# Kernel optimization log

Hardware: AMD Instinct MI355X
Metric: run time of the kernel (lower is better)

The kernel has to match this reference:

```python
import jax, jax.numpy as jnp
import numpy as np

NUM_SEGMENTS = 512
N = 200000
D = 256


def setup_inputs() -> dict:
    key = jax.random.key(0)
    k = jax.random.split(key, 6)
    x = jax.random.normal(k[0], (N, D), dtype=jnp.float32)
    batch = jnp.sort(jax.random.randint(k[1], (N,), 0, NUM_SEGMENTS))
    batch = batch.at[-1].set(NUM_SEGMENTS - 1)  # ensure batch.max()+1 == NUM_SEGMENTS
    W1 = jax.random.normal(k[2], (D, D // 2), dtype=jnp.float32) * (1.0 / np.sqrt(D))
    b1 = jax.random.normal(k[3], (D // 2,), dtype=jnp.float32) * 0.01
    W2 = jax.random.normal(k[4], (D // 2, 1), dtype=jnp.float32) * (1.0 / np.sqrt(D // 2))
    b2 = jax.random.normal(k[5], (1,), dtype=jnp.float32) * 0.01
    return {"x": x, "batch": batch, "W1": W1, "b1": b1, "W2": W2, "b2": b2}


def reference(x, batch, W1, b1, W2, b2):
    # attention MLP: Linear -> Tanh -> Linear -> [N, 1]
    scores = (jnp.tanh(x @ W1 + b1) @ W2 + b2)[:, 0]  # [N]
    # segment softmax (numerically stable): subtract per-segment max
    smax = jax.ops.segment_max(scores, batch, num_segments=NUM_SEGMENTS)  # [G]
    e = jnp.exp(scores - smax[batch])  # [N]
    denom = jax.ops.segment_sum(e, batch, num_segments=NUM_SEGMENTS)  # [G]
    denom = jnp.where(denom > 0, denom, 1.0)  # guard empty segments (original yields zeros)
    w = e / denom[batch]  # [N]
    # weighted sum pooling per segment -> [G, D]
    return jax.ops.segment_sum(x * w[:, None], batch, num_segments=NUM_SEGMENTS)
```

## Files before the change

### kernel.cpp

```cpp
#include <hip/hip_runtime.h>
#include <math.h>


typedef __attribute__((ext_vector_type(4))) float f32x4;
typedef __attribute__((ext_vector_type(8))) short s16x8;

#define MFMA16(A, B, C) __builtin_amdgcn_mfma_f32_16x16x32_bf16((A), (B), (C), 0, 0, 0)

__device__ __forceinline__ unsigned short f2bf_rne(float f) {
    unsigned int u = __float_as_uint(f);
    unsigned int r = u + 0x7FFFu + ((u >> 16) & 1u);
    return (unsigned short)(r >> 16);
}
__device__ __forceinline__ float bf2f(unsigned short h) {
    return __uint_as_float(((unsigned int)h) << 16);
}

#define APITCH 36
#define BPITCH 40

__global__ __launch_bounds__(256)
void scores_mfma(const float* __restrict__ x, const float* __restrict__ W1,
                 const float* __restrict__ b1, const float* __restrict__ W2,
                 const float* __restrict__ b2, float* __restrict__ scores, int N)
{
    __shared__ __align__(16) float Afp[128 * APITCH];
    __shared__ __align__(16) unsigned short Bhi[128 * BPITCH];
    __shared__ __align__(16) unsigned short Blo[128 * BPITCH];

    const int tid  = threadIdx.x;
    const int wave = tid >> 6;
    const int lane = tid & 63;
    const int c    = lane & 15;
    const int q    = lane >> 4;
    const int rowBase = blockIdx.x * 128;

    f32x4 acc[2][8];
#pragma unroll
    for (int mt = 0; mt < 2; ++mt)
#pragma unroll
        for (int nt = 0; nt < 8; ++nt)
            acc[mt][nt] = (f32x4){0.f, 0.f, 0.f, 0.f};

    const int nB   = tid & 127;
    const int half = tid >> 7;

    for (int k0 = 0; k0 < 256; k0 += 32) {
        __syncthreads();
#pragma unroll
        for (int i = 0; i < 4; ++i) {
            int idx = tid + 256 * i;
            int r   = idx >> 3;
            int c4  = idx & 7;
            int row = rowBase + r;
            f32x4 v = (f32x4){0.f, 0.f, 0.f, 0.f};
            if (row < N)
                v = *(const f32x4*)(x + (size_t)row * 256 + k0 + c4 * 4);
            *(f32x4*)&Afp[r * APITCH + c4 * 4] = v;
        }
#pragma unroll
        for (int g = 0; g < 4; ++g) {
            unsigned short hs[4], ls[4];
#pragma unroll
            for (int e = 0; e < 4; ++e) {
                int kk = half * 16 + g * 4 + e;
                float f = W1[(size_t)(k0 + kk) * 128 + nB];
                unsigned short h = f2bf_rne(f);
                hs[e] = h;
                ls[e] = f2bf_rne(f - bf2f(h));
            }
            *(ushort4*)&Bhi[nB * BPITCH + half * 16 + g * 4] =
                make_ushort4(hs[0], hs[1], hs[2], hs[3]);
            *(ushort4*)&Blo[nB * BPITCH + half * 16 + g * 4] =
                make_ushort4(ls[0], ls[1], ls[2], ls[3]);
        }
        __syncthreads();

        s16x8 ahi[2], alo[2];
#pragma unroll
        for (int mt = 0; mt < 2; ++mt) {
            int m = wave * 32 + mt * 16 + c;
            f32x4 a0 = *(const f32x4*)&Afp[m * APITCH + q * 8];
            f32x4 a1 = *(const f32x4*)&Afp[m * APITCH + q * 8 + 4];
            float av[8] = {a0.x, a0.y, a0.z, a0.w, a1.x, a1.y, a1.z, a1.w};
#pragma unroll
            for (int j = 0; j < 8; ++j) {
                unsigned short h = f2bf_rne(av[j]);
                ahi[mt][j] = (short)h;
                alo[mt][j] = (short)f2bf_rne(av[j] - bf2f(h));
            }
        }
#pragma unroll
        for (int nt = 0; nt < 8; ++nt) {
            int nr = nt * 16 + c;
            s16x8 bh = *(const s16x8*)&Bhi[nr * BPITCH + q * 8];
            s16x8 bl = *(const s16x8*)&Blo[nr * BPITCH + q * 8];
#pragma unroll
            for (int mt = 0; mt < 2; ++mt) {
                acc[mt][nt] = MFMA16(ahi[mt], bh, acc[mt][nt]);
                acc[mt][nt] = MFMA16(ahi[mt], bl, acc[mt][nt]);
                acc[mt][nt] = MFMA16(alo[mt], bh, acc[mt][nt]);
            }
        }
    }

    float b1v[8], w2v[8];
#pragma unroll
    for (int nt = 0; nt < 8; ++nt) {
        b1v[nt] = b1[nt * 16 + c];
        w2v[nt] = W2[nt * 16 + c];
    }
    const float bias2 = b2[0];

#pragma unroll
    for (int mt = 0; mt < 2; ++mt) {
#pragma unroll
        for (int reg = 0; reg < 4; ++reg) {
            float p = 0.f;
#pragma unroll
            for (int nt = 0; nt < 8; ++nt) {
                float v = acc[mt][nt][reg] + b1v[nt];
                float e = __expf(2.f * v);
                p += (1.f - 2.f / (e + 1.f)) * w2v[nt];
            }
#pragma unroll
            for (int off = 8; off > 0; off >>= 1)
                p += __shfl_xor(p, off, 16);
            if (c == 0) {
                int row = rowBase + wave * 32 + mt * 16 + q * 4 + reg;
                if (row < N) scores[row] = p + bias2;
            }
        }
    }
}

__device__ __forceinline__ int lower_bound_dev(const int* __restrict__ b, int n, int v)
{
    int lo = 0, hi = n;
    while (lo < hi) {
        int mid = (lo + hi) >> 1;
        if (b[mid] < v) lo = mid + 1; else hi = mid;
    }
    return lo;
}

__global__ __launch_bounds__(1024)
void segpool_kernel(const float* __restrict__ x, const int* __restrict__ batch,
                    const float* __restrict__ scores, float* __restrict__ out, int N)
{
    const int g = blockIdx.x;
    const int tid = threadIdx.x;
    const int fidx  = tid & 63;
    const int rslot = tid >> 6;

    __shared__ int se[2];
    __shared__ float sred[1024];
    __shared__ float4 rbuf[16][64];

    if (tid < 2) se[tid] = lower_bound_dev(batch, N, g + tid);
    __syncthreads();
    const int start = se[0], end = se[1];

    float m = -INFINITY;
    for (int i = start + tid; i < end; i += 1024) m = fmaxf(m, scores[i]);
#pragma unroll
    for (int off = 32; off > 0; off >>= 1) m = fmaxf(m, __shfl_xor(m, off, 64));
    if ((tid & 63) == 0) sred[tid >> 6] = m;
    __syncthreads();
    if (tid < 16) {
        float v = sred[tid];
#pragma unroll
        for (int off = 8; off > 0; off >>= 1) v = fmaxf(v, __shfl_xor(v, off, 16));
        if (tid == 0) sred[0] = v;
    }
    __syncthreads();
    m = sred[0];
    __syncthreads();

    float ssum = 0.f;
    for (int i = start + tid; i < end; i += 1024) ssum += expf(scores[i] - m);
#pragma unroll
    for (int off = 32; off > 0; off >>= 1) ssum += __shfl_xor(ssum, off, 64);
    if ((tid & 63) == 0) sred[tid >> 6] = ssum;
    __syncthreads();
    if (tid < 16) {
        float v = sred[tid];
#pragma unroll
        for (int off = 8; off > 0; off >>= 1) v += __shfl_xor(v, off, 16);
        if (tid == 0) sred[0] = v;
    }
    __syncthreads();
    const float denom = sred[0];
    const float inv = (denom > 0.f) ? 1.f / denom : 0.f;

    float4 acc = make_float4(0.f, 0.f, 0.f, 0.f);
    for (int base = start; base < end; base += 1024) {
        int cnt = min(1024, end - base);
        __syncthreads();
        if (tid < cnt) sred[tid] = expf(scores[base + tid] - m) * inv;
        __syncthreads();
#pragma unroll 2
        for (int j = rslot; j < cnt; j += 16) {
            float w = sred[j];
            float4 v = *(const float4*)(x + (size_t)(base + j) * 256 + fidx * 4);
            acc.x = fmaf(w, v.x, acc.x);
            acc.y = fmaf(w, v.y, acc.y);
            acc.z = fmaf(w, v.z, acc.z);
            acc.w = fmaf(w, v.w, acc.w);
        }
    }

    rbuf[rslot][fidx] = acc;
    __syncthreads();
#pragma unroll
    for (int s = 8; s > 0; s >>= 1) {
        if (rslot < s) {
            float4 o = rbuf[rslot + s][fidx];
            acc.x += o.x; acc.y += o.y; acc.z += o.z; acc.w += o.w;
            rbuf[rslot][fidx] = acc;
        }
        __syncthreads();
    }
    if (rslot == 0)
        ((float4*)out)[(size_t)g * 64 + fidx] = acc;
}

extern "C" void kernel_launch(void* const* d_in, const int* in_sizes, int n_in,
                              void* d_out, int out_size, void* d_ws, size_t ws_size,
                              hipStream_t stream) {
    const float* x     = (const float*)d_in[0];
    const int*   batch = (const int*)  d_in[1];
    const float* W1    = (const float*)d_in[2];
    const float* b1    = (const float*)d_in[3];
    const float* W2    = (const float*)d_in[4];
    const float* b2    = (const float*)d_in[5];
    float* out = (float*)d_out;

    const int N = in_sizes[1];
    const int G = out_size / 256;

    float* scores = (float*)d_ws;

    const int mblocks = (N + 127) / 128;
    scores_mfma<<<mblocks, 256, 0, stream>>>(x, W1, b1, W2, b2, scores, N);
    segpool_kernel<<<G, 1024, 0, stream>>>(x, batch, scores, out, N);
}
```

Measured before the change: 399.8 us.

## Precompute bf16 split of W1 and register-prefetch tiles in scores GEMM

Adds a prep kernel that splits W1 into transposed bf16 hi/lo arrays once, stored temporarily in the output buffer, which segpool later overwrites. The scores kernel now converts x to bf16 hi/lo once per element before staging it in LDS, and prefetches the next K-slice of A and B into registers while MFMAs run. The aim is to remove the repeated per-block W1 conversion and strided loads, and to hide global load latency. In exchange it adds an extra launch and more register pressure under a launch_bounds occupancy hint.

New measurement: 360.3 us. -9.9%, faster.

```diff
diff --git a/kernel.cpp b/kernel.cpp
--- a/kernel.cpp
+++ b/kernel.cpp
@@ -1,9 +1,11 @@
 #include <hip/hip_runtime.h>
+#include <hip/hip_bf16.h>
 #include <math.h>
 
 
 typedef __attribute__((ext_vector_type(4))) float f32x4;
 typedef __attribute__((ext_vector_type(8))) short s16x8;
+typedef __attribute__((ext_vector_type(8))) unsigned short u16x8;
 
 #define MFMA16(A, B, C) __builtin_amdgcn_mfma_f32_16x16x32_bf16((A), (B), (C), 0, 0, 0)
 
@@ -16,17 +18,33 @@
     return __uint_as_float(((unsigned int)h) << 16);
 }
 
-#define APITCH 36
-#define BPITCH 40
-
 __global__ __launch_bounds__(256)
-void scores_mfma(const float* __restrict__ x, const float* __restrict__ W1,
+void prep_w1(const float* __restrict__ W1, unsigned short* __restrict__ bh,
+             unsigned short* __restrict__ bl)
+{
+    for (int idx = blockIdx.x * 256 + threadIdx.x; idx < 128 * 256;
+         idx += gridDim.x * 256) {
+        int n = idx & 127, k = idx >> 7;
+        float f = W1[(size_t)k * 128 + n];
+        unsigned short h = f2bf_rne(f);
+        bh[(size_t)n * 256 + k] = h;
+        bl[(size_t)n * 256 + k] = f2bf_rne(f - bf2f(h));
+    }
+}
+
+#define LPITCH 40
+
+__global__ __launch_bounds__(256, 3)
+void scores_mfma(const float* __restrict__ x,
+                 const unsigned short* __restrict__ bh,
+                 const unsigned short* __restrict__ bl,
                  const float* __restrict__ b1, const float* __restrict__ W2,
                  const float* __restrict__ b2, float* __restrict__ scores, int N)
 {
-    __shared__ __align__(16) float Afp[128 * APITCH];
-    __shared__ __align__(16) unsigned short Bhi[128 * BPITCH];
-    __shared__ __align__(16) unsigned short Blo[128 * BPITCH];
+    __shared__ __align__(16) unsigned short Ahi[128 * LPITCH];
+    __shared__ __align__(16) unsigned short Alo[128 * LPITCH];
+    __shared__ __align__(16) unsigned short Bhi[128 * LPITCH];
+    __shared__ __align__(16) unsigned short Blo[128 * LPITCH];
 
     const int tid  = threadIdx.x;
     const int wave = tid >> 6;
@@ -42,64 +60,89 @@
         for (int nt = 0; nt < 8; ++nt)
             acc[mt][nt] = (f32x4){0.f, 0.f, 0.f, 0.f};
 
-    const int nB   = tid & 127;
-    const int half = tid >> 7;
-
-    for (int k0 = 0; k0 < 256; k0 += 32) {
-        __syncthreads();
-#pragma unroll
-        for (int i = 0; i < 4; ++i) {
-            int idx = tid + 256 * i;
-            int r   = idx >> 3;
-            int c4  = idx & 7;
-            int row = rowBase + r;
-            f32x4 v = (f32x4){0.f, 0.f, 0.f, 0.f};
-            if (row < N)
-                v = *(const f32x4*)(x + (size_t)row * 256 + k0 + c4 * 4);
-            *(f32x4*)&Afp[r * APITCH + c4 * 4] = v;
-        }
-#pragma unroll
-        for (int g = 0; g < 4; ++g) {
-            unsigned short hs[4], ls[4];
-#pragma unroll
-            for (int e = 0; e < 4; ++e) {
-                int kk = half * 16 + g * 4 + e;
-                float f = W1[(size_t)(k0 + kk) * 128 + nB];
-                unsigned short h = f2bf_rne(f);
-                hs[e] = h;
-                ls[e] = f2bf_rne(f - bf2f(h));
-            }
-            *(ushort4*)&Bhi[nB * BPITCH + half * 16 + g * 4] =
-                make_ushort4(hs[0], hs[1], hs[2], hs[3]);
-            *(ushort4*)&Blo[nB * BPITCH + half * 16 + g * 4] =
-                make_ushort4(ls[0], ls[1], ls[2], ls[3]);
-        }
-        __syncthreads();
-
-        s16x8 ahi[2], alo[2];
+    const int arow  = rowBase + (tid >> 1);
+    const int ak16  = (tid & 1) * 16;
+    const int nB    = tid & 127;
+    const int bk16  = (tid >> 7) * 16;
+
+    f32x4 pa0, pa1, pa2, pa3;
+    u16x8 pb0, pb1, pl0, pl1;
+
+    auto loadA = [&](int k0) {
+        if (arow < N) {
+            const float* p = x + (size_t)arow * 256 + k0 + ak16;
+            pa0 = *(const f32x4*)(p);
+            pa1 = *(const f32x4*)(p + 4);
+            pa2 = *(const f32x4*)(p + 8);
+            pa3 = *(const f32x4*)(p + 12);
+        } else {
+            pa0 = pa1 = pa2 = pa3 = (f32x4){0.f, 0.f, 0.f, 0.f};
+        }
+    };
+    auto loadB = [&](int k0) {
+        const size_t base = (size_t)nB * 256 + k0 + bk16;
+        pb0 = *(const u16x8*)(bh + base);
+        pb1 = *(const u16x8*)(bh + base + 8);
+        pl0 = *(const u16x8*)(bl + base);
+        pl1 = *(const u16x8*)(bl + base + 8);
+    };
+
+    loadA(0);
+    loadB(0);
+
+    for (int it = 0; it < 8; ++it) {
+        float af[16];
+        *(f32x4*)&af[0]  = pa0; *(f32x4*)&af[4]  = pa1;
+        *(f32x4*)&af[8]  = pa2; *(f32x4*)&af[12] = pa3;
+        unsigned short ah[16], al[16];
+#pragma unroll
+        for (int j = 0; j < 8; ++j) {
+            float a0 = af[2 * j], a1 = af[2 * j + 1];
+            __hip_bfloat162 h2 = __float22bfloat162_rn(make_float2(a0, a1));
+            ushort2 hu = *(ushort2*)&h2;
+            float r0 = a0 - bf2f(hu.x), r1 = a1 - bf2f(hu.y);
+            __hip_bfloat162 l2 = __float22bfloat162_rn(make_float2(r0, r1));
+            ushort2 lu = *(ushort2*)&l2;
+            ah[2 * j] = hu.x; ah[2 * j + 1] = hu.y;
+            al[2 * j] = lu.x; al[2 * j + 1] = lu.y;
+        }
+
+        __syncthreads();
+        {
+            const int ar = tid >> 1;
+            *(u16x8*)&Ahi[ar * LPITCH + ak16 + 0] = *(u16x8*)&ah[0];
+            *(u16x8*)&Ahi[ar * LPITCH + ak16 + 8] = *(u16x8*)&ah[8];
+            *(u16x8*)&Alo[ar * LPITCH + ak16 + 0] = *(u16x8*)&al[0];
+            *(u16x8*)&Alo[ar * LPITCH + ak16 + 8] = *(u16x8*)&al[8];
+            *(u16x8*)&Bhi[nB * LPITCH + bk16 + 0] = pb0;
+            *(u16x8*)&Bhi[nB * LPITCH + bk16 + 8] = pb1;
+            *(u16x8*)&Blo[nB * LPITCH + bk16 + 0] = pl0;
+            *(u16x8*)&Blo[nB * LPITCH + bk16 + 8] = pl1;
+        }
+        __syncthreads();
+
+        if (it < 7) {
+            loadA((it + 1) * 32);
+            loadB((it + 1) * 32);
+        }
+
+        s16x8 fah[2], fal[2];
 #pragma unroll
         for (int mt = 0; mt < 2; ++mt) {
             int m = wave * 32 + mt * 16 + c;
-            f32x4 a0 = *(const f32x4*)&Afp[m * APITCH + q * 8];
-            f32x4 a1 = *(const f32x4*)&Afp[m * APITCH + q * 8 + 4];
-            float av[8] = {a0.x, a0.y, a0.z, a0.w, a1.x, a1.y, a1.z, a1.w};
-#pragma unroll
-            for (int j = 0; j < 8; ++j) {
-                unsigned short h = f2bf_rne(av[j]);
-                ahi[mt][j] = (short)h;
-                alo[mt][j] = (short)f2bf_rne(av[j] - bf2f(h));
-            }
+            fah[mt] = *(const s16x8*)&Ahi[m * LPITCH + q * 8];
+            fal[mt] = *(const s16x8*)&Alo[m * LPITCH + q * 8];
         }
 #pragma unroll
         for (int nt = 0; nt < 8; ++nt) {
             int nr = nt * 16 + c;
-            s16x8 bh = *(const s16x8*)&Bhi[nr * BPITCH + q * 8];
-            s16x8 bl = *(const s16x8*)&Blo[nr * BPITCH + q * 8];
+            s16x8 fbh = *(const s16x8*)&Bhi[nr * LPITCH + q * 8];
+            s16x8 fbl = *(const s16x8*)&Blo[nr * LPITCH + q * 8];
 #pragma unroll
             for (int mt = 0; mt < 2; ++mt) {
-                acc[mt][nt] = MFMA16(ahi[mt], bh, acc[mt][nt]);
-                acc[mt][nt] = MFMA16(ahi[mt], bl, acc[mt][nt]);
-                acc[mt][nt] = MFMA16(alo[mt], bh, acc[mt][nt]);
+                acc[mt][nt] = MFMA16(fah[mt], fbh, acc[mt][nt]);
+                acc[mt][nt] = MFMA16(fah[mt], fbl, acc[mt][nt]);
+                acc[mt][nt] = MFMA16(fal[mt], fbh, acc[mt][nt]);
             }
         }
     }
@@ -241,7 +284,11 @@
 
     float* scores = (float*)d_ws;
 
+    unsigned short* bh = (unsigned short*)d_out;
+    unsigned short* bl = bh + 128 * 256;
+
+    prep_w1<<<64, 256, 0, stream>>>(W1, bh, bl);
     const int mblocks = (N + 127) / 128;
-    scores_mfma<<<mblocks, 256, 0, stream>>>(x, W1, b1, W2, b2, scores, N);
+    scores_mfma<<<mblocks, 256, 0, stream>>>(x, bh, bl, b1, W2, b2, scores, N);
     segpool_kernel<<<G, 1024, 0, stream>>>(x, batch, scores, out, N);
 }
```
